# Kernel tuning notes

Measured on AMD Instinct MI355X. Metric: run time of the kernel, lower is better.

The kernel has to match this reference:

```python
import jax, jax.numpy as jnp
import numpy as np

EPS = 1e-12  # matches torch F.normalize default eps

def _l2_normalize(v, axis):
    n = jnp.sqrt(jnp.sum(v * v, axis=axis, keepdims=True))
    return v / jnp.maximum(n, EPS)

def setup_inputs() -> dict:
    key = jax.random.key(0)
    k1, k2, k3 = jax.random.split(key, 3)
    N, C, H, W = 16, 128, 64, 64
    D, K = 512, 64
    x = jax.random.normal(k1, (N, C, H, W), dtype=jnp.float32)
    conv_w = jax.random.normal(k2, (D, C), dtype=jnp.float32) * (1.0 / np.sqrt(C))
    conv_b = jnp.zeros((D,), dtype=jnp.float32)
    centroids = jax.random.uniform(k3, (K, D), dtype=jnp.float32)
    return {"x": x, "conv_w": conv_w, "conv_b": conv_b, "centroids": centroids}

def reference(x, conv_w, conv_b, centroids):
    N, C, H, W = x.shape
    D = conv_w.shape[0]
    # descriptor-wise L2 normalization over channels
    x = _l2_normalize(x, axis=1)
    # 1x1 conv == per-pixel linear projection; flatten spatial -> L = H*W
    f = jnp.einsum('nchw,dc->ndhw', x, conv_w) + conv_b[None, :, None, None]
    f = f.reshape(N, D, H * W)                      # (N, D, L)
    c = _l2_normalize(centroids, axis=1)            # (K, D)
    # soft assignment: dot of normalized centroid with each projected descriptor
    logits = jnp.einsum('kd,ndl->nkl', c, f)        # (N, K, L)
    s = jax.nn.softmax(logits, axis=-1)             # softmax over spatial positions
    # weighted sum of descriptors per cluster (no (N,K,D,L) materialization)
    vlad = jnp.einsum('nkl,ndl->nkd', s, f)         # (N, K, D)
    return vlad
```

## Files before the change

### kernel.cpp

```cpp
#include <hip/hip_runtime.h>

#define NB 16
#define CD 128
#define HW 4096
#define DD 512
#define KC 64

typedef __attribute__((ext_vector_type(8))) short bfrag;
typedef __attribute__((ext_vector_type(4))) float facc;

__device__ __forceinline__ unsigned short f2bf(float f) {
  union { float f; unsigned u; } v; v.f = f;
  unsigned r = v.u + 0x7fffu + ((v.u >> 16) & 1u);
  return (unsigned short)(r >> 16);
}
__device__ __forceinline__ float bf2f(unsigned short h) {
  union { unsigned u; float f; } v; v.u = ((unsigned)h) << 16; return v.f;
}
__device__ __forceinline__ unsigned f2bf2(float lo, float hi) {
  unsigned r;
  asm("v_cvt_pk_bf16_f32 %0, %1, %2" : "=v"(r) : "v"(lo), "v"(hi));
  return r;
}
__device__ __forceinline__ void gll16(const void* g, void* l) {
  __builtin_amdgcn_global_load_lds(
      (__attribute__((address_space(1))) void*)(uintptr_t)g,
      (__attribute__((address_space(3))) void*)(uintptr_t)l, 16, 0, 0);
}
__device__ __forceinline__ int swzr(int r) { return ((r & 7) ^ ((r >> 3) & 7)) << 4; }

__global__ __launch_bounds__(256) void k_prep(const float* __restrict__ conv_w,
                                              const float* __restrict__ centroids,
                                              unsigned short* __restrict__ Wsw,
                                              unsigned short* __restrict__ Cbsw) {
  int b = blockIdx.x, t = threadIdx.x;
  if (b < KC) {
    const float* row = centroids + (size_t)b * DD;
    float v0 = row[t], v1 = row[t + 256];
    float ss = v0 * v0 + v1 * v1;
    #pragma unroll
    for (int off = 32; off; off >>= 1) ss += __shfl_xor(ss, off);
    __shared__ float red[4];
    if ((t & 63) == 0) red[t >> 6] = ss;
    __syncthreads();
    float tot = red[0] + red[1] + red[2] + red[3];
    float inv = 1.0f / fmaxf(sqrtf(tot), 1e-12f);
    int d0 = t, d1 = t + 256;
    *(unsigned short*)((char*)Cbsw + (d0 >> 6) * 8192 + b * 128 +
                       (((d0 & 63) * 2) ^ swzr(b))) = f2bf(v0 * inv);
    *(unsigned short*)((char*)Cbsw + (d1 >> 6) * 8192 + b * 128 +
                       (((d1 & 63) * 2) ^ swzr(b))) = f2bf(v1 * inv);
  } else {
    int i = (b - KC) * 2048 + t * 8;
    const float4* src = (const float4*)(conv_w + i);
    float4 a = src[0], c4 = src[1];
    int d = i >> 7, c0 = i & 127;
    int dch = d >> 6, dl = d & 63;
    uint4 w;
    w.x = f2bf2(a.x, a.y);   w.y = f2bf2(a.z, a.w);
    w.z = f2bf2(c4.x, c4.y); w.w = f2bf2(c4.z, c4.w);
    *(uint4*)((char*)Wsw + dch * 16384 + dl * 256 + ((c0 * 2) ^ swzr(dl))) = w;
  }
}

__global__ __launch_bounds__(512, 2) void k_xproj(const float* __restrict__ x,
                                                  const unsigned short* __restrict__ Wsw,
                                                  const unsigned short* __restrict__ Cbsw,
                                                  const float* __restrict__ conv_b,
                                                  unsigned short* __restrict__ fT,
                                                  unsigned short* __restrict__ eg,
                                                  float* __restrict__ psums) {
  __shared__ __align__(16) char smem[67072];
  char* Xraw  = smem;
  char* fbuf  = smem;
  char* etile = smem + 16384;
  char* Ws    = smem + 32768;
  char* Cb2   = smem + 49152;
  float* invb = (float*)(smem + 65536);
  float* ps   = (float*)(smem + 66048);
  int n = blockIdx.y, lblk = blockIdx.x, l0 = lblk * 128;
  int t = threadIdx.x, lane = t & 63, wid = t >> 6;

  #pragma unroll
  for (int q = 0; q < 2; q++)
    gll16((const char*)Wsw + (q * 8 + wid) * 1024 + lane * 16, Ws + (q * 8 + wid) * 1024);
  gll16((const char*)Cbsw + wid * 1024 + lane * 16, Cb2 + wid * 1024);

  #pragma unroll
  for (int j = 0; j < 2; j++) {
    int c0 = ((t >> 4) + 32 * j) * 2;
    const float4* r0p = (const float4*)(x + ((size_t)n * CD + c0) * HW + l0);
    const float4* r1p = (const float4*)(x + ((size_t)n * CD + c0 + 1) * HW + l0);
    #pragma unroll
    for (int jj = 0; jj < 2; jj++) {
      int f4 = (t & 15) + 16 * jj;
      float4 a = r0p[f4], b = r1p[f4];
      int lb = f4 * 4;
      *(unsigned*)(Xraw + (lb + 0) * 256 + ((c0 * 2) ^ swzr(lb + 0))) = f2bf2(a.x, b.x);
      *(unsigned*)(Xraw + (lb + 1) * 256 + ((c0 * 2) ^ swzr(lb + 1))) = f2bf2(a.y, b.y);
      *(unsigned*)(Xraw + (lb + 2) * 256 + ((c0 * 2) ^ swzr(lb + 2))) = f2bf2(a.z, b.z);
      *(unsigned*)(Xraw + (lb + 3) * 256 + ((c0 * 2) ^ swzr(lb + 3))) = f2bf2(a.w, b.w);
    }
  }
  __syncthreads();

  {
    int l = t >> 2;
    float ss = 0.f;
    #pragma unroll
    for (int p = 0; p < 4; p++) {
      int s16 = (t & 3) + 4 * p;
      bfrag v = *(const bfrag*)(Xraw + l * 256 + ((s16 * 16) ^ swzr(l)));
      #pragma unroll
      for (int i = 0; i < 8; i++) { float f = bf2f((unsigned short)v[i]); ss += f * f; }
    }
    ss += __shfl_xor(ss, 1); ss += __shfl_xor(ss, 2);
    if ((t & 3) == 0) invb[l] = 1.0f / fmaxf(sqrtf(ss), 1e-12f);
  }
  __syncthreads();

  int wd = wid & 1, wl = wid >> 1;
  int er = wid >> 2, ec = wid & 3;
  int r0 = (lane >> 4) << 2, cl = lane & 15;
  int hi8 = (lane >> 4) << 3;

  bfrag bfh[4][2];
  #pragma unroll
  for (int kk = 0; kk < 4; kk++)
    #pragma unroll
    for (int j = 0; j < 2; j++) {
      int row = wl * 32 + j * 16 + cl;
      int c0e = kk * 32 + hi8;
      bfh[kk][j] = *(const bfrag*)(Xraw + row * 256 + ((c0e * 2) ^ swzr(row)));
    }
  float hinv[2];
  #pragma unroll
  for (int j = 0; j < 2; j++) hinv[j] = invb[wl * 32 + j * 16 + cl];
  __syncthreads();

  facc zero = {0.f, 0.f, 0.f, 0.f};
  facc e_acc[2][2];
  e_acc[0][0] = zero; e_acc[0][1] = zero; e_acc[1][0] = zero; e_acc[1][1] = zero;

  for (int dch = 0; dch < 8; dch++) {
    const char* Cbs = Cb2 + ((dch & 1) << 13);
    facc acc[2][2];
    acc[0][0] = zero; acc[0][1] = zero; acc[1][0] = zero; acc[1][1] = zero;
    #pragma unroll
    for (int kk = 0; kk < 4; kk++) {
      int c0e = kk * 32 + hi8;
      bfrag am[2];
      #pragma unroll
      for (int m = 0; m < 2; m++) {
        int d = wd * 32 + m * 16 + cl;
        am[m] = *(const bfrag*)(Ws + d * 256 + ((c0e * 2) ^ swzr(d)));
      }
      #pragma unroll
      for (int m = 0; m < 2; m++)
        #pragma unroll
        for (int j = 0; j < 2; j++)
          acc[m][j] = __builtin_amdgcn_mfma_f32_16x16x32_bf16(am[m], bfh[kk][j], acc[m][j], 0, 0, 0);
    }
    #pragma unroll
    for (int m = 0; m < 2; m++) {
      int d0 = wd * 32 + m * 16 + r0;
      float4 bq = *(const float4*)(conv_b + dch * 64 + d0);
      #pragma unroll
      for (int j = 0; j < 2; j++) {
        int l = wl * 32 + j * 16 + cl;
        uint2 w;
        w.x = f2bf2(acc[m][j][0] * hinv[j] + bq.x, acc[m][j][1] * hinv[j] + bq.y);
        w.y = f2bf2(acc[m][j][2] * hinv[j] + bq.z, acc[m][j][3] * hinv[j] + bq.w);
        *(uint2*)(fbuf + l * 128 + ((d0 * 2) ^ swzr(l))) = w;
      }
    }
    asm volatile("s_waitcnt vmcnt(2) lgkmcnt(0)" ::: "memory");
    __builtin_amdgcn_s_barrier();
    __builtin_amdgcn_sched_barrier(0);
    if (dch < 7) {
      #pragma unroll
      for (int q = 0; q < 2; q++)
        gll16((const char*)Wsw + (dch + 1) * 16384 + (q * 8 + wid) * 1024 + lane * 16,
              Ws + (q * 8 + wid) * 1024);
      gll16((const char*)Cbsw + (dch + 1) * 8192 + wid * 1024 + lane * 16,
            Cb2 + (((dch + 1) & 1) << 13) + wid * 1024);
    }
    __builtin_amdgcn_sched_barrier(0);
    {
      #pragma unroll
      for (int p = 0; p < 2; p++) {
        int ch = p * 512 + t;
        int lr = ch >> 3, c16 = ch & 7;
        bfrag v = *(const bfrag*)(fbuf + lr * 128 + ((c16 * 16) ^ swzr(lr)));
        *(bfrag*)(fT + ((size_t)n * HW + l0 + lr) * DD + dch * 64 + c16 * 8) = v;
      }
    }
    #pragma unroll
    for (int kk = 0; kk < 2; kk++) {
      int d0 = kk * 32 + hi8;
      bfrag ca[2], fb[2];
      #pragma unroll
      for (int m2 = 0; m2 < 2; m2++) {
        int k2 = er * 32 + m2 * 16 + cl;
        ca[m2] = *(const bfrag*)(Cbs + k2 * 128 + ((d0 * 2) ^ swzr(k2)));
      }
      #pragma unroll
      for (int j2 = 0; j2 < 2; j2++) {
        int l2 = ec * 32 + j2 * 16 + cl;
        fb[j2] = *(const bfrag*)(fbuf + l2 * 128 + ((d0 * 2) ^ swzr(l2)));
      }
      #pragma unroll
      for (int m2 = 0; m2 < 2; m2++)
        #pragma unroll
        for (int j2 = 0; j2 < 2; j2++)
          e_acc[m2][j2] = __builtin_amdgcn_mfma_f32_16x16x32_bf16(ca[m2], fb[j2], e_acc[m2][j2], 0, 0, 0);
    }
    asm volatile("s_waitcnt vmcnt(3) lgkmcnt(0)" ::: "memory");
    __builtin_amdgcn_s_barrier();
    __builtin_amdgcn_sched_barrier(0);
  }

  {
    int l2base = ec * 32;
    #pragma unroll
    for (int m2 = 0; m2 < 2; m2++) {
      #pragma unroll
      for (int q = 0; q < 4; q++) {
        int k2 = er * 32 + m2 * 16 + r0 + q;
        float vsum = 0.f;
        #pragma unroll
        for (int j2 = 0; j2 < 2; j2++) {
          int l2 = l2base + j2 * 16 + cl;
          float ev = __expf(e_acc[m2][j2][q]);
          *(unsigned short*)(etile + (l2 >> 6) * 8192 + k2 * 128 +
                             (((l2 & 63) * 2) ^ swzr(k2))) = f2bf(ev);
          vsum += ev;
        }
        vsum += __shfl_xor(vsum, 1); vsum += __shfl_xor(vsum, 2);
        vsum += __shfl_xor(vsum, 4); vsum += __shfl_xor(vsum, 8);
        if (cl == 0) ps[k2 * 4 + ec] = vsum;
      }
    }
  }
  __syncthreads();
  {
    size_t base = ((size_t)n * 64 + lblk * 2) * 8192;
    #pragma unroll
    for (int p = 0; p < 2; p++) {
      uint4 v = *(const uint4*)(etile + (t + p * 512) * 16);
      *(uint4*)((char*)eg + base + (t + p * 512) * 16) = v;
    }
  }
  if (t < 64) {
    float4 v = ((const float4*)ps)[t];
    psums[((size_t)n * 32 + lblk) * 64 + t] = v.x + v.y + v.z + v.w;
  }
}

__global__ __launch_bounds__(256, 2) void k_vlad(const unsigned short* __restrict__ eg,
                                                 const unsigned short* __restrict__ fT,
                                                 float* __restrict__ part) {
  __shared__ __align__(16) char smem[49152];
  char* As = smem;
  char* Bs = smem + 16384;
  int t = threadIdx.x, lane = t & 63, wid = t >> 6;
  int wr = wid >> 1, wc = wid & 1;
  int lin = blockIdx.x;
  int xcd = lin & 7, jj = lin >> 3;
  int grp = xcd * 16 + (jj >> 2);
  int dt = jj & 3, n = grp >> 3, sk = grp & 7;
  int dbase = dt * 128;
  const unsigned short* fTb = fT + (size_t)n * HW * DD + dbase;
  facc acc[2][4];
  facc zero = {0.f, 0.f, 0.f, 0.f};
  #pragma unroll
  for (int m = 0; m < 2; m++)
    #pragma unroll
    for (int j = 0; j < 4; j++) acc[m][j] = zero;

  bfrag br[8];
  #pragma unroll
  for (int q = 0; q < 8; q++) {
    int ch = q * 256 + t;
    int l = ch >> 4, dc = ch & 15;
    br[q] = *(const bfrag*)(fTb + (size_t)(sk * 512 + l) * DD + dc * 8);
  }

  #pragma unroll
  for (int ks = 0; ks < 4; ks++) {
    int l0 = sk * 512 + ks * 128;
    #pragma unroll
    for (int q = 0; q < 8; q++) {
      int ch = q * 256 + t;
      int l = ch >> 4, dc = ch & 15;
      #pragma unroll
      for (int i = 0; i < 8; i++) {
        int d = dc * 8 + i;
        int swz = (((d & 7) ^ ((d >> 3) & 7)) << 4);
        *(unsigned short*)(Bs + d * 256 + ((l * 2) ^ swz)) = (unsigned short)br[q][i];
      }
    }
    __builtin_amdgcn_sched_barrier(0);
    {
      const char* easrc = (const char*)eg + ((size_t)n * 64 + (l0 >> 6)) * 8192;
      #pragma unroll
      for (int q = 0; q < 4; q++)
        gll16(easrc + (q * 4 + wid) * 1024 + lane * 16, As + (q * 4 + wid) * 1024);
    }
    __builtin_amdgcn_sched_barrier(0);
    if (ks < 3) {
      #pragma unroll
      for (int q = 0; q < 8; q++) {
        int ch = q * 256 + t;
        int l = ch >> 4, dc = ch & 15;
        br[q] = *(const bfrag*)(fTb + (size_t)(l0 + 128 + l) * DD + dc * 8);
      }
      asm volatile("s_waitcnt vmcnt(8) lgkmcnt(0)" ::: "memory");
    } else {
      asm volatile("s_waitcnt vmcnt(0) lgkmcnt(0)" ::: "memory");
    }
    __builtin_amdgcn_s_barrier();
    __builtin_amdgcn_sched_barrier(0);
    #pragma unroll
    for (int kk = 0; kk < 128; kk += 32) {
      int lk = kk + ((lane >> 4) << 3);
      const char* Ai = As + (kk >> 6) * 8192;
      int ll = lk & 63;
      bfrag af[2], bf[4];
      #pragma unroll
      for (int m = 0; m < 2; m++) {
        int krow = wr * 32 + m * 16 + (lane & 15);
        af[m] = *(const bfrag*)(Ai + krow * 128 + ((ll * 2) ^ swzr(krow)));
      }
      #pragma unroll
      for (int j = 0; j < 4; j++) {
        int d = wc * 64 + j * 16 + (lane & 15);
        int swz = (((d & 7) ^ ((d >> 3) & 7)) << 4);
        bf[j] = *(const bfrag*)(Bs + d * 256 + ((lk * 2) ^ swz));
      }
      #pragma unroll
      for (int m = 0; m < 2; m++)
        #pragma unroll
        for (int j = 0; j < 4; j++)
          acc[m][j] = __builtin_amdgcn_mfma_f32_16x16x32_bf16(af[m], bf[j], acc[m][j], 0, 0, 0);
    }
    asm volatile("s_waitcnt lgkmcnt(0)" ::: "memory");
    __builtin_amdgcn_s_barrier();
    __builtin_amdgcn_sched_barrier(0);
  }
  int r0 = (lane >> 4) << 2, cl = lane & 15;
  size_t base = ((size_t)(sk * NB + n)) * (KC * DD);
  #pragma unroll
  for (int m = 0; m < 2; m++) {
    int krow = wr * 32 + m * 16 + r0;
    #pragma unroll
    for (int j = 0; j < 4; j++) {
      int d = dbase + wc * 64 + j * 16 + cl;
      #pragma unroll
      for (int q = 0; q < 4; q++)
        part[base + (size_t)(krow + q) * DD + d] = acc[m][j][q];
    }
  }
}

__global__ __launch_bounds__(256) void k_reduce(const float* __restrict__ part,
                                                const float* __restrict__ psums,
                                                float* __restrict__ out) {
  int b = blockIdx.x, t = threadIdx.x;
  int nk = b >> 1;
  int n = nk >> 6, k = nk & 63;
  __shared__ float rsh;
  if (t < 32) {
    float s = psums[((size_t)n * 32 + t) * 64 + k];
    #pragma unroll
    for (int off = 16; off; off >>= 1) s += __shfl_xor(s, off, 32);
    if (t == 0) rsh = 1.0f / s;
  }
  __syncthreads();
  float rinv = rsh;
  int i = b * 256 + t;
  float s = 0.f;
  #pragma unroll
  for (int skk = 0; skk < 8; skk++) s += part[(size_t)skk * (NB * KC * DD) + i];
  out[i] = s * rinv;
}

extern "C" void kernel_launch(void* const* d_in, const int* in_sizes, int n_in,
                              void* d_out, int out_size, void* d_ws, size_t ws_size,
                              hipStream_t stream) {
  const float* x         = (const float*)d_in[0];
  const float* conv_w    = (const float*)d_in[1];
  const float* conv_b    = (const float*)d_in[2];
  const float* centroids = (const float*)d_in[3];
  float* out = (float*)d_out;
  char* ws = (char*)d_ws;

  unsigned short* Wsw  = (unsigned short*)(ws);
  unsigned short* Cbsw = (unsigned short*)(ws + 131072);
  unsigned short* fT   = (unsigned short*)(ws + 196608);
  unsigned short* eg   = (unsigned short*)(ws + 67305472ull);
  float*          psums= (float*)(ws + 75694080ull);
  float*          part = (float*)(ws + 75960320ull);

  k_prep<<<dim3(96), dim3(256), 0, stream>>>(conv_w, centroids, Wsw, Cbsw);

  k_xproj<<<dim3(32, NB), dim3(512), 0, stream>>>(x, Wsw, Cbsw, conv_b, fT, eg, psums);

  k_vlad<<<dim3(512), dim3(256), 0, stream>>>(eg, fT, part);

  k_reduce<<<dim3(NB * KC * DD / 256), dim3(256), 0, stream>>>(part, psums, out);

  (void)in_sizes; (void)n_in; (void)out_size; (void)ws_size;
}
```

Baseline: 54.78 us.

## Precompute centroid-projected weights so logits come straight from normalized input

Folds the centroid matrix into the 1x1 conv weights (M = C·W, bias bk = C·b) in a new small prep kernel, so logits are computed as M·x scaled by the inverse norm plus bk directly from the input tile, rather than from the projected bf16 features. This removes the per-chunk logit MFMA work and the centroid tile loads from the main loop. The freed LDS is used to double-buffer both the weight tiles and the feature output buffer, and each chunk's feature stores are deferred by one iteration to overlap them with compute. It adds an extra kernel launch and changes rounding, since logits no longer pass through bf16-rounded features.

```diff
diff --git a/kernel.cpp b/kernel.cpp
--- a/kernel.cpp
+++ b/kernel.cpp
@@ -32,7 +32,7 @@
 __global__ __launch_bounds__(256) void k_prep(const float* __restrict__ conv_w,
                                               const float* __restrict__ centroids,
                                               unsigned short* __restrict__ Wsw,
-                                              unsigned short* __restrict__ Cbsw) {
+                                              unsigned short* __restrict__ Cb) {
   int b = blockIdx.x, t = threadIdx.x;
   if (b < KC) {
     const float* row = centroids + (size_t)b * DD;
@@ -45,11 +45,8 @@
     __syncthreads();
     float tot = red[0] + red[1] + red[2] + red[3];
     float inv = 1.0f / fmaxf(sqrtf(tot), 1e-12f);
-    int d0 = t, d1 = t + 256;
-    *(unsigned short*)((char*)Cbsw + (d0 >> 6) * 8192 + b * 128 +
-                       (((d0 & 63) * 2) ^ swzr(b))) = f2bf(v0 * inv);
-    *(unsigned short*)((char*)Cbsw + (d1 >> 6) * 8192 + b * 128 +
-                       (((d1 & 63) * 2) ^ swzr(b))) = f2bf(v1 * inv);
+    Cb[(size_t)b * DD + t]       = f2bf(v0 * inv);
+    Cb[(size_t)b * DD + t + 256] = f2bf(v1 * inv);
   } else {
     int i = (b - KC) * 2048 + t * 8;
     const float4* src = (const float4*)(conv_w + i);
@@ -63,19 +60,45 @@
   }
 }
 
+__global__ __launch_bounds__(256) void k_prepM(const float* __restrict__ conv_w,
+                                               const float* __restrict__ conv_b,
+                                               const unsigned short* __restrict__ Cb,
+                                               unsigned short* __restrict__ Mg,
+                                               float* __restrict__ bk) {
+  int b = blockIdx.x, t = threadIdx.x;
+  if (b < 32) {
+    int id = b * 256 + t;
+    int k = id >> 7, c = id & 127;
+    const unsigned short* cbr = Cb + (size_t)k * DD;
+    float m0 = 0.f, m1 = 0.f, m2 = 0.f, m3 = 0.f;
+    #pragma unroll 4
+    for (int d = 0; d < DD; d += 4) {
+      m0 += bf2f(cbr[d + 0]) * conv_w[(size_t)(d + 0) * CD + c];
+      m1 += bf2f(cbr[d + 1]) * conv_w[(size_t)(d + 1) * CD + c];
+      m2 += bf2f(cbr[d + 2]) * conv_w[(size_t)(d + 2) * CD + c];
+      m3 += bf2f(cbr[d + 3]) * conv_w[(size_t)(d + 3) * CD + c];
+    }
+    Mg[id] = f2bf((m0 + m1) + (m2 + m3));
+  } else if (t < KC) {
+    const unsigned short* cbr = Cb + (size_t)t * DD;
+    float s = 0.f;
+    for (int d = 0; d < DD; d++) s += bf2f(cbr[d]) * conv_b[d];
+    bk[t] = s;
+  }
+}
+
 __global__ __launch_bounds__(512, 2) void k_xproj(const float* __restrict__ x,
                                                   const unsigned short* __restrict__ Wsw,
-                                                  const unsigned short* __restrict__ Cbsw,
+                                                  const unsigned short* __restrict__ Mg,
+                                                  const float* __restrict__ bk,
                                                   const float* __restrict__ conv_b,
                                                   unsigned short* __restrict__ fT,
                                                   unsigned short* __restrict__ eg,
                                                   float* __restrict__ psums) {
   __shared__ __align__(16) char smem[67072];
   char* Xraw  = smem;
-  char* fbuf  = smem;
-  char* etile = smem + 16384;
-  char* Ws    = smem + 32768;
-  char* Cb2   = smem + 49152;
+  char* etile = smem;
+  char* Ws0   = smem + 32768;
   float* invb = (float*)(smem + 65536);
   float* ps   = (float*)(smem + 66048);
   int n = blockIdx.y, lblk = blockIdx.x, l0 = lblk * 128;
@@ -83,8 +106,7 @@
 
   #pragma unroll
   for (int q = 0; q < 2; q++)
-    gll16((const char*)Wsw + (q * 8 + wid) * 1024 + lane * 16, Ws + (q * 8 + wid) * 1024);
-  gll16((const char*)Cbsw + wid * 1024 + lane * 16, Cb2 + wid * 1024);
+    gll16((const char*)Wsw + (q * 8 + wid) * 1024 + lane * 16, Ws0 + (q * 8 + wid) * 1024);
 
   #pragma unroll
   for (int j = 0; j < 2; j++) {
@@ -104,6 +126,18 @@
   }
   __syncthreads();
 
+  int wd = wid & 1, wl = wid >> 1;
+  int ek = wid & 1;
+  int r0 = (lane >> 4) << 2, cl = lane & 15;
+  int hi8 = (lane >> 4) << 3;
+
+  bfrag ma[4][2];
+  #pragma unroll
+  for (int kk = 0; kk < 4; kk++)
+    #pragma unroll
+    for (int m2 = 0; m2 < 2; m2++)
+      ma[kk][m2] = *(const bfrag*)(Mg + (size_t)(ek * 32 + m2 * 16 + cl) * CD + kk * 32 + hi8);
+
   {
     int l = t >> 2;
     float ss = 0.f;
@@ -118,11 +152,6 @@
     if ((t & 3) == 0) invb[l] = 1.0f / fmaxf(sqrtf(ss), 1e-12f);
   }
   __syncthreads();
-
-  int wd = wid & 1, wl = wid >> 1;
-  int er = wid >> 2, ec = wid & 3;
-  int r0 = (lane >> 4) << 2, cl = lane & 15;
-  int hi8 = (lane >> 4) << 3;
 
   bfrag bfh[4][2];
   #pragma unroll
@@ -141,9 +170,17 @@
   facc zero = {0.f, 0.f, 0.f, 0.f};
   facc e_acc[2][2];
   e_acc[0][0] = zero; e_acc[0][1] = zero; e_acc[1][0] = zero; e_acc[1][1] = zero;
+  #pragma unroll
+  for (int kk = 0; kk < 4; kk++)
+    #pragma unroll
+    for (int m2 = 0; m2 < 2; m2++)
+      #pragma unroll
+      for (int j2 = 0; j2 < 2; j2++)
+        e_acc[m2][j2] = __builtin_amdgcn_mfma_f32_16x16x32_bf16(ma[kk][m2], bfh[kk][j2], e_acc[m2][j2], 0, 0, 0);
 
   for (int dch = 0; dch < 8; dch++) {
-    const char* Cbs = Cb2 + ((dch & 1) << 13);
+    const char* Wsb = Ws0 + ((dch & 1) << 14);
+    char* fb = smem + ((dch & 1) << 14);
     facc acc[2][2];
     acc[0][0] = zero; acc[0][1] = zero; acc[1][0] = zero; acc[1][1] = zero;
     #pragma unroll
@@ -153,7 +190,7 @@
       #pragma unroll
       for (int m = 0; m < 2; m++) {
         int d = wd * 32 + m * 16 + cl;
-        am[m] = *(const bfrag*)(Ws + d * 256 + ((c0e * 2) ^ swzr(d)));
+        am[m] = *(const bfrag*)(Wsb + d * 256 + ((c0e * 2) ^ swzr(d)));
       }
       #pragma unroll
       for (int m = 0; m < 2; m++)
@@ -171,74 +208,63 @@
         uint2 w;
         w.x = f2bf2(acc[m][j][0] * hinv[j] + bq.x, acc[m][j][1] * hinv[j] + bq.y);
         w.y = f2bf2(acc[m][j][2] * hinv[j] + bq.z, acc[m][j][3] * hinv[j] + bq.w);
-        *(uint2*)(fbuf + l * 128 + ((d0 * 2) ^ swzr(l))) = w;
-      }
-    }
-    asm volatile("s_waitcnt vmcnt(2) lgkmcnt(0)" ::: "memory");
-    __builtin_amdgcn_s_barrier();
-    __builtin_amdgcn_sched_barrier(0);
+        *(uint2*)(fb + l * 128 + ((d0 * 2) ^ swzr(l))) = w;
+      }
+    }
     if (dch < 7) {
       #pragma unroll
       for (int q = 0; q < 2; q++)
         gll16((const char*)Wsw + (dch + 1) * 16384 + (q * 8 + wid) * 1024 + lane * 16,
-              Ws + (q * 8 + wid) * 1024);
-      gll16((const char*)Cbsw + (dch + 1) * 8192 + wid * 1024 + lane * 16,
-            Cb2 + (((dch + 1) & 1) << 13) + wid * 1024);
-    }
-    __builtin_amdgcn_sched_barrier(0);
-    {
+              Ws0 + (((dch + 1) & 1) << 14) + (q * 8 + wid) * 1024);
+    }
+    __builtin_amdgcn_sched_barrier(0);
+    if (dch >= 1) {
+      const char* fprev = smem + (((dch - 1) & 1) << 14);
       #pragma unroll
       for (int p = 0; p < 2; p++) {
         int ch = p * 512 + t;
         int lr = ch >> 3, c16 = ch & 7;
-        bfrag v = *(const bfrag*)(fbuf + lr * 128 + ((c16 * 16) ^ swzr(lr)));
-        *(bfrag*)(fT + ((size_t)n * HW + l0 + lr) * DD + dch * 64 + c16 * 8) = v;
-      }
-    }
-    #pragma unroll
-    for (int kk = 0; kk < 2; kk++) {
-      int d0 = kk * 32 + hi8;
-      bfrag ca[2], fb[2];
-      #pragma unroll
-      for (int m2 = 0; m2 < 2; m2++) {
-        int k2 = er * 32 + m2 * 16 + cl;
-        ca[m2] = *(const bfrag*)(Cbs + k2 * 128 + ((d0 * 2) ^ swzr(k2)));
-      }
-      #pragma unroll
-      for (int j2 = 0; j2 < 2; j2++) {
-        int l2 = ec * 32 + j2 * 16 + cl;
-        fb[j2] = *(const bfrag*)(fbuf + l2 * 128 + ((d0 * 2) ^ swzr(l2)));
-      }
-      #pragma unroll
-      for (int m2 = 0; m2 < 2; m2++)
-        #pragma unroll
-        for (int j2 = 0; j2 < 2; j2++)
-          e_acc[m2][j2] = __builtin_amdgcn_mfma_f32_16x16x32_bf16(ca[m2], fb[j2], e_acc[m2][j2], 0, 0, 0);
-    }
-    asm volatile("s_waitcnt vmcnt(3) lgkmcnt(0)" ::: "memory");
+        bfrag v = *(const bfrag*)(fprev + lr * 128 + ((c16 * 16) ^ swzr(lr)));
+        *(bfrag*)(fT + ((size_t)n * HW + l0 + lr) * DD + (dch - 1) * 64 + c16 * 8) = v;
+      }
+    }
+    if (dch == 0) { asm volatile("s_waitcnt vmcnt(0) lgkmcnt(0)" ::: "memory"); }
+    else         { asm volatile("s_waitcnt vmcnt(2) lgkmcnt(0)" ::: "memory"); }
     __builtin_amdgcn_s_barrier();
     __builtin_amdgcn_sched_barrier(0);
   }
-
   {
-    int l2base = ec * 32;
+    const char* fprev = smem + 16384;
+    #pragma unroll
+    for (int p = 0; p < 2; p++) {
+      int ch = p * 512 + t;
+      int lr = ch >> 3, c16 = ch & 7;
+      bfrag v = *(const bfrag*)(fprev + lr * 128 + ((c16 * 16) ^ swzr(lr)));
+      *(bfrag*)(fT + ((size_t)n * HW + l0 + lr) * DD + 7 * 64 + c16 * 8) = v;
+    }
+  }
+
+  {
     #pragma unroll
     for (int m2 = 0; m2 < 2; m2++) {
+      int k20 = ek * 32 + m2 * 16 + r0;
+      float4 bkq = *(const float4*)(bk + k20);
       #pragma unroll
       for (int q = 0; q < 4; q++) {
-        int k2 = er * 32 + m2 * 16 + r0 + q;
+        int k2 = k20 + q;
+        float bkv = (q == 0) ? bkq.x : (q == 1) ? bkq.y : (q == 2) ? bkq.z : bkq.w;
         float vsum = 0.f;
         #pragma unroll
         for (int j2 = 0; j2 < 2; j2++) {
-          int l2 = l2base + j2 * 16 + cl;
-          float ev = __expf(e_acc[m2][j2][q]);
+          int l2 = wl * 32 + j2 * 16 + cl;
+          float ev = __expf(e_acc[m2][j2][q] * hinv[j2] + bkv);
           *(unsigned short*)(etile + (l2 >> 6) * 8192 + k2 * 128 +
                              (((l2 & 63) * 2) ^ swzr(k2))) = f2bf(ev);
           vsum += ev;
         }
         vsum += __shfl_xor(vsum, 1); vsum += __shfl_xor(vsum, 2);
         vsum += __shfl_xor(vsum, 4); vsum += __shfl_xor(vsum, 8);
-        if (cl == 0) ps[k2 * 4 + ec] = vsum;
+        if (cl == 0) ps[k2 * 4 + wl] = vsum;
       }
     }
   }
@@ -396,15 +422,18 @@
   char* ws = (char*)d_ws;
 
   unsigned short* Wsw  = (unsigned short*)(ws);
-  unsigned short* Cbsw = (unsigned short*)(ws + 131072);
-  unsigned short* fT   = (unsigned short*)(ws + 196608);
-  unsigned short* eg   = (unsigned short*)(ws + 67305472ull);
-  float*          psums= (float*)(ws + 75694080ull);
-  float*          part = (float*)(ws + 75960320ull);
-
-  k_prep<<<dim3(96), dim3(256), 0, stream>>>(conv_w, centroids, Wsw, Cbsw);
-
-  k_xproj<<<dim3(32, NB), dim3(512), 0, stream>>>(x, Wsw, Cbsw, conv_b, fT, eg, psums);
+  unsigned short* Cb   = (unsigned short*)(ws + 131072);
+  unsigned short* Mg   = (unsigned short*)(ws + 196608);
+  float*          bk   = (float*)(ws + 212992);
+  unsigned short* fT   = (unsigned short*)(ws + 214016);
+  unsigned short* eg   = (unsigned short*)(ws + 67322880ull);
+  float*          psums= (float*)(ws + 75711744ull);
+  float*          part = (float*)(ws + 75842816ull);
+
+  k_prep<<<dim3(96), dim3(256), 0, stream>>>(conv_w, centroids, Wsw, Cb);
+  k_prepM<<<dim3(33), dim3(256), 0, stream>>>(conv_w, conv_b, Cb, Mg, bk);
+
+  k_xproj<<<dim3(32, NB), dim3(512), 0, stream>>>(x, Wsw, Mg, bk, conv_b, fT, eg, psums);
 
   k_vlad<<<dim3(512), dim3(256), 0, stream>>>(eg, fT, part);
 
```

Result: slower. 66.95 us (+22.2%).
